# Optimization experiments

Measured on AMD Instinct MI355X. Metric: run time of the kernel, lower is better.

## Reference

```python
import jax, jax.numpy as jnp
import numpy as np

D_MODEL = 1024
N_EXPERTS = 8
HIDDEN = ((int(round(D_MODEL * (8.0 / 3.0))) + 63) // 64) * 64  # 2752
ALPHA = 0.05  # load_balance_alpha


def setup_inputs() -> dict:
    key = jax.random.key(0)
    ks = jax.random.split(key, 6)
    s = 0.02
    x = jax.random.normal(ks[0], (4, 1024, D_MODEL), dtype=jnp.float32)
    Wg = jax.random.normal(ks[1], (D_MODEL, N_EXPERTS), dtype=jnp.float32) * s
    bg = jnp.zeros((N_EXPERTS,), dtype=jnp.float32)
    Wu = jax.random.normal(ks[2], (N_EXPERTS, D_MODEL, HIDDEN), dtype=jnp.float32) * s
    Wv = jax.random.normal(ks[3], (N_EXPERTS, D_MODEL, HIDDEN), dtype=jnp.float32) * s
    Wd = jax.random.normal(ks[4], (N_EXPERTS, HIDDEN, D_MODEL), dtype=jnp.float32) * s
    return {"x": x, "Wg": Wg, "bg": bg, "Wu": Wu, "Wv": Wv, "Wd": Wd}


def reference(x, Wg, bg, Wu, Wv, Wd):
    b, t, d = x.shape
    E = Wu.shape[0]
    xf = x.reshape(b * t, d)  # [N, d]

    # Top-1 router
    logits = xf @ Wg + bg                      # [N, E]
    probs = jax.nn.softmax(logits, axis=-1)
    top1_idx = jnp.argmax(probs, axis=-1)      # [N]
    top1_p = jnp.max(probs, axis=-1)           # [N]
    onehot = jax.nn.one_hot(top1_idx, E, dtype=x.dtype)  # [N, E]

    # Load-balancing aux loss (both me and ce are under no_grad in the original)
    me = jax.lax.stop_gradient(onehot.mean(axis=0))
    ce = jax.lax.stop_gradient(probs.mean(axis=0))
    aux = ALPHA * E * jnp.sum(me * ce)

    # Dropless dispatch: masked per-expert SwiGLU (loop over small fixed E)
    gate = onehot * top1_p[:, None]            # [N, E] combine weights
    y = jnp.zeros_like(xf)
    for e in range(E):
        u = xf @ Wu[e]                         # [N, H]
        v = xf @ Wv[e]                         # [N, H]
        ye = (jax.nn.silu(u) * v) @ Wd[e]      # [N, d]
        y = y + gate[:, e, None] * ye

    return y.reshape(b, t, d), aux
```

## Files before the change

kernel.cpp:

```cpp
#include <hip/hip_runtime.h>

#define D_MODEL 1024
#define HID     2752
#define NEXP    8
#define NTOK    4096
#define ALPHA   0.05f

typedef __bf16 bf16_t;
typedef bf16_t bf16x8 __attribute__((ext_vector_type(8)));
typedef float  f32x4  __attribute__((ext_vector_type(4)));

__device__ inline unsigned short f2bf(float f) {
    unsigned int u = __float_as_uint(f);
    u += 0x7fffu + ((u >> 16) & 1u);
    return (unsigned short)(u >> 16);
}

__device__ inline bf16x8 ldsFrag(const unsigned short* p) {
    union { uint4 u; bf16x8 b; } t;
    t.u = *(const uint4*)p;
    return t.b;
}

__device__ inline void gload_lds16(const void* g, void* l) {
    __builtin_amdgcn_global_load_lds((const __attribute__((address_space(1))) void*)g,
                                     (__attribute__((address_space(3))) void*)l, 16, 0, 0);
}

__global__ void tobf16_kernel(const float* __restrict__ x, unsigned short* __restrict__ xbf) {
    int i = (blockIdx.x * 256 + threadIdx.x) * 8;
    float4 a = *(const float4*)(x + i);
    float4 b = *(const float4*)(x + i + 4);
    uint4 o;
    o.x = (unsigned)f2bf(a.x) | ((unsigned)f2bf(a.y) << 16);
    o.y = (unsigned)f2bf(a.z) | ((unsigned)f2bf(a.w) << 16);
    o.z = (unsigned)f2bf(b.x) | ((unsigned)f2bf(b.y) << 16);
    o.w = (unsigned)f2bf(b.z) | ((unsigned)f2bf(b.w) << 16);
    *(uint4*)(xbf + i) = o;
}

__global__ __launch_bounds__(256) void transpose_kernel(const float* __restrict__ in,
                                                        unsigned short* __restrict__ out,
                                                        int R, int C) {
    __shared__ float tile[64 * 65];
    const int e = blockIdx.z;
    const float* src = in + (size_t)e * R * C;
    unsigned short* dst = out + (size_t)e * R * C;
    const int c0 = blockIdx.x * 64, r0 = blockIdx.y * 64;
    const int tid = threadIdx.x;
#pragma unroll
    for (int j = 0; j < 4; ++j) {
        int f = j * 256 + tid;
        int row = f >> 4, c4 = f & 15;
        float4 v = *(const float4*)(src + (size_t)(r0 + row) * C + c0 + c4 * 4);
        float* t = &tile[row * 65 + c4 * 4];
        t[0] = v.x; t[1] = v.y; t[2] = v.z; t[3] = v.w;
    }
    __syncthreads();
#pragma unroll
    for (int j = 0; j < 2; ++j) {
        int f = j * 256 + tid;
        int orow = f >> 3, kc = f & 7;
        unsigned short pk[8];
#pragma unroll
        for (int q = 0; q < 8; ++q) pk[q] = f2bf(tile[(kc * 8 + q) * 65 + orow]);
        *(uint4*)(dst + (size_t)(c0 + orow) * R + r0 + kc * 8) = *(uint4*)pk;
    }
}

__global__ void router_kernel(const float* __restrict__ x, const float* __restrict__ Wg,
                              const float* __restrict__ bg,
                              int* __restrict__ eidx, float* __restrict__ gate_p,
                              int* __restrict__ counts, float* __restrict__ ce_sum) {
    __shared__ float ceS[8];
    __shared__ int   cntS[8];
    int tid = threadIdx.x;
    if (tid < 8) { ceS[tid] = 0.f; cntS[tid] = 0; }
    __syncthreads();

    int wid = tid >> 6, lane = tid & 63;
    int t = blockIdx.x * 16 + wid;
    const float* xr = x + (size_t)t * D_MODEL;

    float acc[8];
#pragma unroll
    for (int e = 0; e < 8; ++e) acc[e] = 0.f;

#pragma unroll
    for (int c = 0; c < 4; ++c) {
        int i0 = c * 256 + lane * 4;
        float4 xv = *(const float4*)(xr + i0);
#pragma unroll
        for (int j = 0; j < 4; ++j) {
            const float* wr = Wg + (size_t)(i0 + j) * 8;
            float4 lo = *(const float4*)(wr);
            float4 hi = *(const float4*)(wr + 4);
            float xs = (&xv.x)[j];
            acc[0] += xs * lo.x; acc[1] += xs * lo.y;
            acc[2] += xs * lo.z; acc[3] += xs * lo.w;
            acc[4] += xs * hi.x; acc[5] += xs * hi.y;
            acc[6] += xs * hi.z; acc[7] += xs * hi.w;
        }
    }
#pragma unroll
    for (int e = 0; e < 8; ++e) {
#pragma unroll
        for (int off = 32; off > 0; off >>= 1)
            acc[e] += __shfl_xor(acc[e], off, 64);
    }

    if (lane == 0) {
        float lg[8];
#pragma unroll
        for (int e = 0; e < 8; ++e) lg[e] = acc[e] + bg[e];
        float mx = lg[0]; int am = 0;
#pragma unroll
        for (int e = 1; e < 8; ++e) { if (lg[e] > mx) { mx = lg[e]; am = e; } }
        float ex[8], s = 0.f;
#pragma unroll
        for (int e = 0; e < 8; ++e) { ex[e] = __expf(lg[e] - mx); s += ex[e]; }
        float inv = 1.f / s;
#pragma unroll
        for (int e = 0; e < 8; ++e) atomicAdd(&ceS[e], ex[e] * inv);
        atomicAdd(&cntS[am], 1);
        eidx[t] = am;
        gate_p[t] = ex[am] * inv;
    }
    __syncthreads();
    if (tid < 8) atomicAdd(&ce_sum[tid], ceS[tid]);
    if (tid >= 8 && tid < 16) atomicAdd(&counts[tid - 8], cntS[tid - 8]);
}

__global__ void offsets_aux_kernel(const int* __restrict__ counts, const float* __restrict__ ce_sum,
                                   int* __restrict__ offs, float* __restrict__ aux_out) {
    if (threadIdx.x == 0) {
        int off = 0; float aux = 0.f;
        for (int e = 0; e < 8; ++e) {
            offs[e] = off; off += counts[e];
            aux += ((float)counts[e] / (float)NTOK) * (ce_sum[e] / (float)NTOK);
        }
        aux_out[0] = ALPHA * (float)NEXP * aux;
    }
}

__global__ void scatter_kernel(const int* __restrict__ eidx, const int* __restrict__ offs,
                               int* __restrict__ fill, int* __restrict__ toks) {
    int t = blockIdx.x * 256 + threadIdx.x;
    int e = eidx[t];
    int pos = atomicAdd(&fill[e], 1);
    toks[offs[e] + pos] = t;
}

__global__ __launch_bounds__(256, 2) void gemm1_kernel(
    const unsigned short* __restrict__ WuT, const unsigned short* __restrict__ WvT,
    const unsigned short* __restrict__ xbf,
    const int* __restrict__ toks, const int* __restrict__ counts, const int* __restrict__ offs,
    unsigned short* __restrict__ hbuf) {
    const int e = blockIdx.z;
    const int Ne = counts[e];
    const int mt = blockIdx.y;
    if (mt * 128 >= Ne) return;
    const int nt = blockIdx.x;
    const int slot0 = offs[e] + mt * 128;
    const int rowsV = min(128, Ne - mt * 128);
    const int ncol0 = nt * 128;
    const int colsV = min(128, HID - ncol0);

    __shared__ unsigned short As[128 * 64];
    __shared__ unsigned short Bus[128 * 64];
    __shared__ unsigned short Bvs[128 * 64];

    const int tid = threadIdx.x;

    const unsigned short* aS[4];
    const unsigned short* buS[4];
    const unsigned short* bvS[4];
    unsigned short* aD[4];
    unsigned short* buD[4];
    unsigned short* bvD[4];
#pragma unroll
    for (int i = 0; i < 4; ++i) {
        int c = i * 256 + tid;
        int r = c >> 3, ch = c & 7;
        int srcOff = ((ch ^ (r & 7)) * 8);
        int ar = min(r, rowsV - 1);
        int tok = toks[slot0 + ar];
        aS[i] = xbf + (size_t)tok * D_MODEL + srcOff;
        int bn = ncol0 + min(r, colsV - 1);
        buS[i] = WuT + ((size_t)e * HID + bn) * D_MODEL + srcOff;
        bvS[i] = WvT + ((size_t)e * HID + bn) * D_MODEL + srcOff;
        aD[i]  = As  + c * 8;
        buD[i] = Bus + c * 8;
        bvD[i] = Bvs + c * 8;
    }

    f32x4 accU[4][4], accV[4][4];
#pragma unroll
    for (int m = 0; m < 4; ++m)
#pragma unroll
        for (int n = 0; n < 4; ++n) {
            accU[m][n] = (f32x4){0.f, 0.f, 0.f, 0.f};
            accV[m][n] = (f32x4){0.f, 0.f, 0.f, 0.f};
        }

    const int lane = tid & 63;
    const int w = tid >> 6;
    const int rbase = (w >> 1) * 64;
    const int cbase = (w & 1) * 64;
    const int lrow = lane & 15;
    const int lchunk = lane >> 4;

    for (int ks = 0; ks < 16; ++ks) {
#pragma unroll
        for (int i = 0; i < 4; ++i) gload_lds16(aS[i],  aD[i]);
#pragma unroll
        for (int i = 0; i < 4; ++i) gload_lds16(buS[i], buD[i]);
#pragma unroll
        for (int i = 0; i < 4; ++i) gload_lds16(bvS[i], bvD[i]);
#pragma unroll
        for (int i = 0; i < 4; ++i) { aS[i] += 64; buS[i] += 64; bvS[i] += 64; }
        __syncthreads();

#pragma unroll
        for (int kk = 0; kk < 2; ++kk) {
            const int g = kk * 4 + lchunk;
            bf16x8 af[4], bu[4], bv[4];
#pragma unroll
            for (int m = 0; m < 4; ++m) {
                int r = rbase + m * 16 + lrow;
                af[m] = ldsFrag(&As[r * 64 + ((g ^ (r & 7)) * 8)]);
            }
#pragma unroll
            for (int n = 0; n < 4; ++n) {
                int rn = cbase + n * 16 + lrow;
                int off = rn * 64 + ((g ^ (rn & 7)) * 8);
                bu[n] = ldsFrag(&Bus[off]);
                bv[n] = ldsFrag(&Bvs[off]);
            }
#pragma unroll
            for (int m = 0; m < 4; ++m)
#pragma unroll
                for (int n = 0; n < 4; ++n) {
                    accU[m][n] = __builtin_amdgcn_mfma_f32_16x16x32_bf16(af[m], bu[n], accU[m][n], 0, 0, 0);
                    accV[m][n] = __builtin_amdgcn_mfma_f32_16x16x32_bf16(af[m], bv[n], accV[m][n], 0, 0, 0);
                }
        }
        __syncthreads();
    }

#pragma unroll
    for (int m = 0; m < 4; ++m) {
#pragma unroll
        for (int i = 0; i < 4; ++i) {
            int r = rbase + m * 16 + (lane >> 4) * 4 + i;
            if (r >= rowsV) continue;
            size_t rowOff = (size_t)(slot0 + r) * HID + ncol0;
#pragma unroll
            for (int n = 0; n < 4; ++n) {
                int c = cbase + n * 16 + (lane & 15);
                if (c < colsV) {
                    float u = accU[m][n][i];
                    float v = accV[m][n][i];
                    float s = u / (1.f + __expf(-u));
                    hbuf[rowOff + c] = f2bf(s * v);
                }
            }
        }
    }
}

__global__ __launch_bounds__(256, 3) void gemm2_kernel(
    const unsigned short* __restrict__ WdT, const unsigned short* __restrict__ hbuf,
    const int* __restrict__ toks, const int* __restrict__ counts, const int* __restrict__ offs,
    const float* __restrict__ gate_p, float* __restrict__ yout) {
    const int e = blockIdx.z;
    const int Ne = counts[e];
    const int mt = blockIdx.y;
    if (mt * 128 >= Ne) return;
    const int nt = blockIdx.x;
    const int slot0 = offs[e] + mt * 128;
    const int rowsV = min(128, Ne - mt * 128);
    const int ncol0 = nt * 128;

    __shared__ unsigned short As[128 * 64];
    __shared__ unsigned short Bs[128 * 64];

    const int tid = threadIdx.x;

    const unsigned short* aS[4];
    const unsigned short* bS[4];
    unsigned short* aD[4];
    unsigned short* bD[4];
#pragma unroll
    for (int i = 0; i < 4; ++i) {
        int c = i * 256 + tid;
        int r = c >> 3, ch = c & 7;
        int srcOff = ((ch ^ (r & 7)) * 8);
        int ar = min(r, rowsV - 1);
        aS[i] = hbuf + (size_t)(slot0 + ar) * HID + srcOff;
        bS[i] = WdT + ((size_t)e * D_MODEL + ncol0 + r) * HID + srcOff;
        aD[i] = As + c * 8;
        bD[i] = Bs + c * 8;
    }

    f32x4 acc[4][4];
#pragma unroll
    for (int m = 0; m < 4; ++m)
#pragma unroll
        for (int n = 0; n < 4; ++n) acc[m][n] = (f32x4){0.f, 0.f, 0.f, 0.f};

    const int lane = tid & 63;
    const int w = tid >> 6;
    const int rbase = (w >> 1) * 64;
    const int cbase = (w & 1) * 64;
    const int lrow = lane & 15;
    const int lchunk = lane >> 4;

    for (int ks = 0; ks < 43; ++ks) {
#pragma unroll
        for (int i = 0; i < 4; ++i) gload_lds16(aS[i], aD[i]);
#pragma unroll
        for (int i = 0; i < 4; ++i) gload_lds16(bS[i], bD[i]);
#pragma unroll
        for (int i = 0; i < 4; ++i) { aS[i] += 64; bS[i] += 64; }
        __syncthreads();

#pragma unroll
        for (int kk = 0; kk < 2; ++kk) {
            const int g = kk * 4 + lchunk;
            bf16x8 af[4], bf[4];
#pragma unroll
            for (int m = 0; m < 4; ++m) {
                int r = rbase + m * 16 + lrow;
                af[m] = ldsFrag(&As[r * 64 + ((g ^ (r & 7)) * 8)]);
            }
#pragma unroll
            for (int n = 0; n < 4; ++n) {
                int rn = cbase + n * 16 + lrow;
                bf[n] = ldsFrag(&Bs[rn * 64 + ((g ^ (rn & 7)) * 8)]);
            }
#pragma unroll
            for (int m = 0; m < 4; ++m)
#pragma unroll
                for (int n = 0; n < 4; ++n)
                    acc[m][n] = __builtin_amdgcn_mfma_f32_16x16x32_bf16(af[m], bf[n], acc[m][n], 0, 0, 0);
        }
        __syncthreads();
    }

#pragma unroll
    for (int m = 0; m < 4; ++m) {
#pragma unroll
        for (int i = 0; i < 4; ++i) {
            int r = rbase + m * 16 + (lane >> 4) * 4 + i;
            if (r >= rowsV) continue;
            int tok = toks[slot0 + r];
            float p = gate_p[tok];
            float* yrow = yout + (size_t)tok * D_MODEL + ncol0;
#pragma unroll
            for (int n = 0; n < 4; ++n) {
                int c = cbase + n * 16 + (lane & 15);
                yrow[c] = p * acc[m][n][i];
            }
        }
    }
}

extern "C" void kernel_launch(void* const* d_in, const int* in_sizes, int n_in,
                              void* d_out, int out_size, void* d_ws, size_t ws_size,
                              hipStream_t stream) {
    const float* x  = (const float*)d_in[0];
    const float* Wg = (const float*)d_in[1];
    const float* bg = (const float*)d_in[2];
    const float* Wu = (const float*)d_in[3];
    const float* Wv = (const float*)d_in[4];
    const float* Wd = (const float*)d_in[5];
    float* yout = (float*)d_out;
    float* aux_out = yout + (size_t)NTOK * D_MODEL;

    char* ws = (char*)d_ws;
    int*   counts = (int*)(ws + 0);
    int*   offs   = (int*)(ws + 32);
    float* ce_sum = (float*)(ws + 64);
    int*   fill   = (int*)(ws + 96);
    int*   eidx   = (int*)(ws + 128);
    float* gate_p = (float*)(ws + 16512);
    int*   toks   = (int*)(ws + 32896);
    unsigned short* xbf  = (unsigned short*)(ws + 65536);
    unsigned short* hbuf = (unsigned short*)(ws + 8454144);
    unsigned short* WuT  = (unsigned short*)(ws + 30998528);
    unsigned short* WvT  = (unsigned short*)(ws + 76087296);
    unsigned short* WdT  = WuT;

    hipMemsetAsync(ws, 0, 128, stream);
    tobf16_kernel<<<2048, 256, 0, stream>>>(x, xbf);
    router_kernel<<<256, 1024, 0, stream>>>(x, Wg, bg, eidx, gate_p, counts, ce_sum);
    offsets_aux_kernel<<<1, 64, 0, stream>>>(counts, ce_sum, offs, aux_out);
    scatter_kernel<<<16, 256, 0, stream>>>(eidx, offs, fill, toks);
    transpose_kernel<<<dim3(HID / 64, D_MODEL / 64, 8), 256, 0, stream>>>(Wu, WuT, D_MODEL, HID);
    transpose_kernel<<<dim3(HID / 64, D_MODEL / 64, 8), 256, 0, stream>>>(Wv, WvT, D_MODEL, HID);
    gemm1_kernel<<<dim3(22, 32, 8), 256, 0, stream>>>(WuT, WvT, xbf, toks, counts, offs, hbuf);
    transpose_kernel<<<dim3(D_MODEL / 64, HID / 64, 8), 256, 0, stream>>>(Wd, WdT, HID, D_MODEL);
    gemm2_kernel<<<dim3(8, 32, 8), 256, 0, stream>>>(WdT, hbuf, toks, counts, offs, gate_p, yout);
}
```

Baseline: 283.5 us.

## Use 512-thread GEMM blocks, double-buffer gemm2 LDS, merge Wu/Wv transposes

Both expert GEMMs now run 512-thread blocks (8 waves, each owning a 64x32 sub-tile) instead of 256 threads, and the grid is reordered so M-tiles vary fastest. gemm2 gains double-buffered LDS so the next K-slice loads while MFMAs run on the current one. The separate Wu and Wv transpose launches are merged into one kernel over a grid of 16 z-slices. Together these aim to improve latency hiding and cut one launch, at the cost of more LDS per gemm2 block and possibly lower occupancy.

```diff
diff --git a/kernel.cpp b/kernel.cpp
--- a/kernel.cpp
+++ b/kernel.cpp
@@ -39,6 +39,37 @@
     *(uint4*)(xbf + i) = o;
 }
 
+__global__ __launch_bounds__(256) void transposeUV_kernel(const float* __restrict__ Wu,
+                                                          const float* __restrict__ Wv,
+                                                          unsigned short* __restrict__ WuT,
+                                                          unsigned short* __restrict__ WvT) {
+    __shared__ float tile[64 * 65];
+    const int z = blockIdx.z;
+    const int e = z & 7;
+    const float* src = ((z < 8) ? Wu : Wv) + (size_t)e * D_MODEL * HID;
+    unsigned short* dst = ((z < 8) ? WuT : WvT) + (size_t)e * D_MODEL * HID;
+    const int c0 = blockIdx.x * 64, r0 = blockIdx.y * 64;
+    const int tid = threadIdx.x;
+#pragma unroll
+    for (int j = 0; j < 4; ++j) {
+        int f = j * 256 + tid;
+        int row = f >> 4, c4 = f & 15;
+        float4 v = *(const float4*)(src + (size_t)(r0 + row) * HID + c0 + c4 * 4);
+        float* t = &tile[row * 65 + c4 * 4];
+        t[0] = v.x; t[1] = v.y; t[2] = v.z; t[3] = v.w;
+    }
+    __syncthreads();
+#pragma unroll
+    for (int j = 0; j < 2; ++j) {
+        int f = j * 256 + tid;
+        int orow = f >> 3, kc = f & 7;
+        unsigned short pk[8];
+#pragma unroll
+        for (int q = 0; q < 8; ++q) pk[q] = f2bf(tile[(kc * 8 + q) * 65 + orow]);
+        *(uint4*)(dst + (size_t)(c0 + orow) * D_MODEL + r0 + kc * 8) = *(uint4*)pk;
+    }
+}
+
 __global__ __launch_bounds__(256) void transpose_kernel(const float* __restrict__ in,
                                                         unsigned short* __restrict__ out,
                                                         int R, int C) {
@@ -151,16 +182,16 @@
     toks[offs[e] + pos] = t;
 }
 
-__global__ __launch_bounds__(256, 2) void gemm1_kernel(
+__global__ __launch_bounds__(512, 4) void gemm1_kernel(
     const unsigned short* __restrict__ WuT, const unsigned short* __restrict__ WvT,
     const unsigned short* __restrict__ xbf,
     const int* __restrict__ toks, const int* __restrict__ counts, const int* __restrict__ offs,
     unsigned short* __restrict__ hbuf) {
     const int e = blockIdx.z;
     const int Ne = counts[e];
-    const int mt = blockIdx.y;
+    const int mt = blockIdx.x;
     if (mt * 128 >= Ne) return;
-    const int nt = blockIdx.x;
+    const int nt = blockIdx.y;
     const int slot0 = offs[e] + mt * 128;
     const int rowsV = min(128, Ne - mt * 128);
     const int ncol0 = nt * 128;
@@ -172,17 +203,13 @@
 
     const int tid = threadIdx.x;
 
-    const unsigned short* aS[4];
-    const unsigned short* buS[4];
-    const unsigned short* bvS[4];
-    unsigned short* aD[4];
-    unsigned short* buD[4];
-    unsigned short* bvD[4];
-#pragma unroll
-    for (int i = 0; i < 4; ++i) {
-        int c = i * 256 + tid;
+    const unsigned short *aS[2], *buS[2], *bvS[2];
+    unsigned short *aD[2], *buD[2], *bvD[2];
+#pragma unroll
+    for (int i = 0; i < 2; ++i) {
+        int c = i * 512 + tid;
         int r = c >> 3, ch = c & 7;
-        int srcOff = ((ch ^ (r & 7)) * 8);
+        int srcOff = (ch ^ (r & 7)) * 8;
         int ar = min(r, rowsV - 1);
         int tok = toks[slot0 + ar];
         aS[i] = xbf + (size_t)tok * D_MODEL + srcOff;
@@ -194,44 +221,44 @@
         bvD[i] = Bvs + c * 8;
     }
 
-    f32x4 accU[4][4], accV[4][4];
+    f32x4 accU[4][2], accV[4][2];
 #pragma unroll
     for (int m = 0; m < 4; ++m)
 #pragma unroll
-        for (int n = 0; n < 4; ++n) {
+        for (int n = 0; n < 2; ++n) {
             accU[m][n] = (f32x4){0.f, 0.f, 0.f, 0.f};
             accV[m][n] = (f32x4){0.f, 0.f, 0.f, 0.f};
         }
 
     const int lane = tid & 63;
     const int w = tid >> 6;
-    const int rbase = (w >> 1) * 64;
-    const int cbase = (w & 1) * 64;
+    const int rbase = (w >> 2) * 64;
+    const int cbase = (w & 3) * 32;
     const int lrow = lane & 15;
     const int lchunk = lane >> 4;
 
     for (int ks = 0; ks < 16; ++ks) {
 #pragma unroll
-        for (int i = 0; i < 4; ++i) gload_lds16(aS[i],  aD[i]);
-#pragma unroll
-        for (int i = 0; i < 4; ++i) gload_lds16(buS[i], buD[i]);
-#pragma unroll
-        for (int i = 0; i < 4; ++i) gload_lds16(bvS[i], bvD[i]);
-#pragma unroll
-        for (int i = 0; i < 4; ++i) { aS[i] += 64; buS[i] += 64; bvS[i] += 64; }
+        for (int i = 0; i < 2; ++i) gload_lds16(aS[i],  aD[i]);
+#pragma unroll
+        for (int i = 0; i < 2; ++i) gload_lds16(buS[i], buD[i]);
+#pragma unroll
+        for (int i = 0; i < 2; ++i) gload_lds16(bvS[i], bvD[i]);
+#pragma unroll
+        for (int i = 0; i < 2; ++i) { aS[i] += 64; buS[i] += 64; bvS[i] += 64; }
         __syncthreads();
 
 #pragma unroll
         for (int kk = 0; kk < 2; ++kk) {
             const int g = kk * 4 + lchunk;
-            bf16x8 af[4], bu[4], bv[4];
+            bf16x8 af[4], bu[2], bv[2];
 #pragma unroll
             for (int m = 0; m < 4; ++m) {
                 int r = rbase + m * 16 + lrow;
                 af[m] = ldsFrag(&As[r * 64 + ((g ^ (r & 7)) * 8)]);
             }
 #pragma unroll
-            for (int n = 0; n < 4; ++n) {
+            for (int n = 0; n < 2; ++n) {
                 int rn = cbase + n * 16 + lrow;
                 int off = rn * 64 + ((g ^ (rn & 7)) * 8);
                 bu[n] = ldsFrag(&Bus[off]);
@@ -240,7 +267,7 @@
 #pragma unroll
             for (int m = 0; m < 4; ++m)
 #pragma unroll
-                for (int n = 0; n < 4; ++n) {
+                for (int n = 0; n < 2; ++n) {
                     accU[m][n] = __builtin_amdgcn_mfma_f32_16x16x32_bf16(af[m], bu[n], accU[m][n], 0, 0, 0);
                     accV[m][n] = __builtin_amdgcn_mfma_f32_16x16x32_bf16(af[m], bv[n], accV[m][n], 0, 0, 0);
                 }
@@ -256,7 +283,7 @@
             if (r >= rowsV) continue;
             size_t rowOff = (size_t)(slot0 + r) * HID + ncol0;
 #pragma unroll
-            for (int n = 0; n < 4; ++n) {
+            for (int n = 0; n < 2; ++n) {
                 int c = cbase + n * 16 + (lane & 15);
                 if (c < colsV) {
                     float u = accU[m][n][i];
@@ -269,83 +296,90 @@
     }
 }
 
-__global__ __launch_bounds__(256, 3) void gemm2_kernel(
+__global__ __launch_bounds__(512, 4) void gemm2_kernel(
     const unsigned short* __restrict__ WdT, const unsigned short* __restrict__ hbuf,
     const int* __restrict__ toks, const int* __restrict__ counts, const int* __restrict__ offs,
     const float* __restrict__ gate_p, float* __restrict__ yout) {
     const int e = blockIdx.z;
     const int Ne = counts[e];
-    const int mt = blockIdx.y;
+    const int mt = blockIdx.x;
     if (mt * 128 >= Ne) return;
-    const int nt = blockIdx.x;
+    const int nt = blockIdx.y;
     const int slot0 = offs[e] + mt * 128;
     const int rowsV = min(128, Ne - mt * 128);
     const int ncol0 = nt * 128;
 
-    __shared__ unsigned short As[128 * 64];
-    __shared__ unsigned short Bs[128 * 64];
+    __shared__ unsigned short As[2][128 * 64];
+    __shared__ unsigned short Bs[2][128 * 64];
 
     const int tid = threadIdx.x;
 
-    const unsigned short* aS[4];
-    const unsigned short* bS[4];
-    unsigned short* aD[4];
-    unsigned short* bD[4];
-#pragma unroll
-    for (int i = 0; i < 4; ++i) {
-        int c = i * 256 + tid;
+    const unsigned short *aS[2], *bS[2];
+    int off8[2];
+#pragma unroll
+    for (int i = 0; i < 2; ++i) {
+        int c = i * 512 + tid;
         int r = c >> 3, ch = c & 7;
-        int srcOff = ((ch ^ (r & 7)) * 8);
+        int srcOff = (ch ^ (r & 7)) * 8;
         int ar = min(r, rowsV - 1);
         aS[i] = hbuf + (size_t)(slot0 + ar) * HID + srcOff;
         bS[i] = WdT + ((size_t)e * D_MODEL + ncol0 + r) * HID + srcOff;
-        aD[i] = As + c * 8;
-        bD[i] = Bs + c * 8;
-    }
-
-    f32x4 acc[4][4];
+        off8[i] = c * 8;
+    }
+
+    f32x4 acc[4][2];
 #pragma unroll
     for (int m = 0; m < 4; ++m)
 #pragma unroll
-        for (int n = 0; n < 4; ++n) acc[m][n] = (f32x4){0.f, 0.f, 0.f, 0.f};
+        for (int n = 0; n < 2; ++n) acc[m][n] = (f32x4){0.f, 0.f, 0.f, 0.f};
 
     const int lane = tid & 63;
     const int w = tid >> 6;
-    const int rbase = (w >> 1) * 64;
-    const int cbase = (w & 1) * 64;
+    const int rbase = (w >> 2) * 64;
+    const int cbase = (w & 3) * 32;
     const int lrow = lane & 15;
     const int lchunk = lane >> 4;
 
+#pragma unroll
+    for (int i = 0; i < 2; ++i) {
+        gload_lds16(aS[i], &As[0][off8[i]]);
+        gload_lds16(bS[i], &Bs[0][off8[i]]);
+        aS[i] += 64; bS[i] += 64;
+    }
+    __syncthreads();
+
+    int cur = 0;
     for (int ks = 0; ks < 43; ++ks) {
-#pragma unroll
-        for (int i = 0; i < 4; ++i) gload_lds16(aS[i], aD[i]);
-#pragma unroll
-        for (int i = 0; i < 4; ++i) gload_lds16(bS[i], bD[i]);
-#pragma unroll
-        for (int i = 0; i < 4; ++i) { aS[i] += 64; bS[i] += 64; }
-        __syncthreads();
-
+        if (ks < 42) {
+#pragma unroll
+            for (int i = 0; i < 2; ++i) {
+                gload_lds16(aS[i], &As[cur ^ 1][off8[i]]);
+                gload_lds16(bS[i], &Bs[cur ^ 1][off8[i]]);
+                aS[i] += 64; bS[i] += 64;
+            }
+        }
 #pragma unroll
         for (int kk = 0; kk < 2; ++kk) {
             const int g = kk * 4 + lchunk;
-            bf16x8 af[4], bf[4];
+            bf16x8 af[4], bf[2];
 #pragma unroll
             for (int m = 0; m < 4; ++m) {
                 int r = rbase + m * 16 + lrow;
-                af[m] = ldsFrag(&As[r * 64 + ((g ^ (r & 7)) * 8)]);
-            }
-#pragma unroll
-            for (int n = 0; n < 4; ++n) {
+                af[m] = ldsFrag(&As[cur][r * 64 + ((g ^ (r & 7)) * 8)]);
+            }
+#pragma unroll
+            for (int n = 0; n < 2; ++n) {
                 int rn = cbase + n * 16 + lrow;
-                bf[n] = ldsFrag(&Bs[rn * 64 + ((g ^ (rn & 7)) * 8)]);
+                bf[n] = ldsFrag(&Bs[cur][rn * 64 + ((g ^ (rn & 7)) * 8)]);
             }
 #pragma unroll
             for (int m = 0; m < 4; ++m)
 #pragma unroll
-                for (int n = 0; n < 4; ++n)
+                for (int n = 0; n < 2; ++n)
                     acc[m][n] = __builtin_amdgcn_mfma_f32_16x16x32_bf16(af[m], bf[n], acc[m][n], 0, 0, 0);
         }
         __syncthreads();
+        cur ^= 1;
     }
 
 #pragma unroll
@@ -358,7 +392,7 @@
             float p = gate_p[tok];
             float* yrow = yout + (size_t)tok * D_MODEL + ncol0;
 #pragma unroll
-            for (int n = 0; n < 4; ++n) {
+            for (int n = 0; n < 2; ++n) {
                 int c = cbase + n * 16 + (lane & 15);
                 yrow[c] = p * acc[m][n][i];
             }
@@ -397,9 +431,8 @@
     router_kernel<<<256, 1024, 0, stream>>>(x, Wg, bg, eidx, gate_p, counts, ce_sum);
     offsets_aux_kernel<<<1, 64, 0, stream>>>(counts, ce_sum, offs, aux_out);
     scatter_kernel<<<16, 256, 0, stream>>>(eidx, offs, fill, toks);
-    transpose_kernel<<<dim3(HID / 64, D_MODEL / 64, 8), 256, 0, stream>>>(Wu, WuT, D_MODEL, HID);
-    transpose_kernel<<<dim3(HID / 64, D_MODEL / 64, 8), 256, 0, stream>>>(Wv, WvT, D_MODEL, HID);
-    gemm1_kernel<<<dim3(22, 32, 8), 256, 0, stream>>>(WuT, WvT, xbf, toks, counts, offs, hbuf);
+    transposeUV_kernel<<<dim3(HID / 64, D_MODEL / 64, 16), 256, 0, stream>>>(Wu, Wv, WuT, WvT);
+    gemm1_kernel<<<dim3(32, 22, 8), 512, 0, stream>>>(WuT, WvT, xbf, toks, counts, offs, hbuf);
     transpose_kernel<<<dim3(D_MODEL / 64, HID / 64, 8), 256, 0, stream>>>(Wd, WdT, HID, D_MODEL);
-    gemm2_kernel<<<dim3(8, 32, 8), 256, 0, stream>>>(WdT, hbuf, toks, counts, offs, gate_p, yout);
-}
+    gemm2_kernel<<<dim3(32, 8, 8), 512, 0, stream>>>(WdT, hbuf, toks, counts, offs, gate_p, yout);
+}
```

New measurement: 853.8 us. 3.01x slower.
